# Optimization experiments

Hardware: AMD Instinct MI355X
Metric: run time of the kernel (lower is better)

Reference implementation:

```python
import jax, jax.numpy as jnp
import numpy as np

EPS = 1e-5
DC = 4  # conv kernel size


def _rmsnorm(x, w):
    return x * jax.lax.rsqrt(jnp.mean(x * x, axis=-1, keepdims=True) + EPS) * w


def _depthwise_causal_conv(x, w, b):
    # x: (B, L, ED), w: (ED, 1, DC), b: (ED,)
    xt = jnp.transpose(x, (0, 2, 1))  # (B, ED, L)
    y = jax.lax.conv_general_dilated(
        xt, w, window_strides=(1,), padding=[(DC - 1, 0)],
        feature_group_count=w.shape[0], dimension_numbers=("NCH", "OIH", "NCH"))
    y = y + b[None, :, None]
    return jnp.transpose(y, (0, 2, 1))  # (B, L, ED)


def _mamba_block(x, in_w, cw, cb, xp_w, dt_w, dt_b, A_log, Dp, out_w):
    B, L, _ = x.shape
    ED, N = A_log.shape
    dt_rank = dt_w.shape[1]
    xz = jnp.einsum('bld,ed->ble', x, in_w)          # (B, L, 2*ED)
    xi, z = jnp.split(xz, 2, axis=-1)
    xi = jax.nn.silu(_depthwise_causal_conv(xi, cw, cb))  # (B, L, ED)
    dbc = jnp.einsum('ble,fe->blf', xi, xp_w)        # (B, L, dt_rank+2N)
    delta, Bm, Cm = jnp.split(dbc, [dt_rank, dt_rank + N], axis=-1)
    delta = jax.nn.softplus(jnp.einsum('blr,er->ble', delta, dt_w) + dt_b)  # (B,L,ED)
    A = -jnp.exp(A_log)                              # (ED, N)
    dA = jnp.exp(delta[..., None] * A)               # (B, L, ED, N)
    dBx = delta[..., None] * Bm[:, :, None, :] * xi[..., None]  # (B, L, ED, N)

    def step(h, inp):
        a, bx = inp
        h = a * h + bx
        return h, h

    h0 = jnp.zeros((B, ED, N), x.dtype)
    _, hs = jax.lax.scan(step, h0, (jnp.moveaxis(dA, 1, 0), jnp.moveaxis(dBx, 1, 0)))
    y = jnp.einsum('lbdn,bln->bld', hs, Cm) + Dp * xi  # (B, L, ED)
    y = y * jax.nn.silu(z)
    return jnp.einsum('ble,de->bld', y, out_w)


def setup_inputs() -> dict:
    key = jax.random.key(0)
    ks = jax.random.split(key, 12)
    B, L, Dm, NL, ED, N, R = 16, 2048, 64, 4, 128, 16, 4
    s = 0.05
    A = jnp.tile(jnp.log(jnp.arange(1, N + 1, dtype=jnp.float32))[None, None, :], (NL, ED, 1))
    return {
        "x": jax.random.normal(ks[0], (B, L, Dm), jnp.float32),
        "norm_w": jnp.ones((NL, Dm), jnp.float32),
        "in_proj_w": jax.random.normal(ks[1], (NL, 2 * ED, Dm), jnp.float32) * s,
        "conv_w": jax.random.normal(ks[2], (NL, ED, 1, DC), jnp.float32) * 0.2,
        "conv_b": jnp.zeros((NL, ED), jnp.float32),
        "x_proj_w": jax.random.normal(ks[3], (NL, R + 2 * N, ED), jnp.float32) * s,
        "dt_proj_w": jax.random.normal(ks[4], (NL, ED, R), jnp.float32) * s,
        "dt_proj_b": jnp.full((NL, ED), -4.0, jnp.float32),
        "A_log": A,
        "D_skip": jnp.ones((NL, ED), jnp.float32),
        "out_proj_w": jax.random.normal(ks[5], (NL, Dm, ED), jnp.float32) * s,
        "fc_w": jax.random.normal(ks[6], (Dm, Dm), jnp.float32) * s,
        "fc_b": jnp.zeros((Dm,), jnp.float32),
    }


def reference(x, norm_w, in_proj_w, conv_w, conv_b, x_proj_w, dt_proj_w,
              dt_proj_b, A_log, D_skip, out_proj_w, fc_w, fc_b):
    n_layers = norm_w.shape[0]
    for l in range(n_layers):
        x = x + _mamba_block(_rmsnorm(x, norm_w[l]), in_proj_w[l], conv_w[l],
                             conv_b[l], x_proj_w[l], dt_proj_w[l], dt_proj_b[l],
                             A_log[l], D_skip[l], out_proj_w[l])
    last = x[:, -1, :]
    return jnp.einsum('bd,od->bo', last, fc_w) + fc_b
```

## Files before the change

kernel.cpp:

```cpp
#include <hip/hip_runtime.h>
#include <math.h>

#define B_   16
#define L_   2048
#define DM   64
#define NL_  4
#define ED_  128
#define NS   16
#define RK   4
#define BL   (B_*L_)
#define CHUNKS 128
#define CHLEN  (L_/CHUNKS)
#define SEQS   (B_*ED_*NS)

__device__ __forceinline__ void pow_chain16(float r, float* p) {
  float r2 = r * r, r4 = r2 * r2, r8 = r4 * r4;
  p[0]=r;      p[1]=r2;      p[2]=r2*r;    p[3]=r4;
  p[4]=r4*r;   p[5]=r4*r2;   p[6]=r4*p[2]; p[7]=r8;
  p[8]=r8*r;   p[9]=r8*r2;   p[10]=r8*p[2];p[11]=r8*r4;
  p[12]=r8*p[4];p[13]=r8*p[5];p[14]=r8*p[6];p[15]=r8*r8;
}

__global__ __launch_bounds__(256) void gemm_in_rms_k(const float* __restrict__ X,
    const float* __restrict__ nw, const float* __restrict__ W, float* __restrict__ XZ)
{
  __shared__ float4 sX[64][17];
  __shared__ float4 sW[16][64];
  int tid = threadIdx.x;
  int row0 = blockIdx.x * 64;
  int col0 = blockIdx.y * 64;
  const float* Wh = W + (size_t)col0 * 64;
#pragma unroll
  for (int it = 0; it < 4; it++) {
    int i = tid + it * 256;
    int r = i >> 4, q = i & 15;
    float4 v = *(const float4*)(X + (size_t)(row0 + r) * 64 + q * 4);
    float ss = v.x*v.x + v.y*v.y + v.z*v.z + v.w*v.w;
    ss += __shfl_xor(ss, 1, 16);
    ss += __shfl_xor(ss, 2, 16);
    ss += __shfl_xor(ss, 4, 16);
    ss += __shfl_xor(ss, 8, 16);
    float sc = rsqrtf(ss * (1.0f/64.0f) + 1e-5f);
    float4 wv = *(const float4*)(nw + q * 4);
    float4 o;
    o.x = v.x*sc*wv.x; o.y = v.y*sc*wv.y; o.z = v.z*sc*wv.z; o.w = v.w*sc*wv.w;
    sX[r][q] = o;
  }
#pragma unroll
  for (int it = 0; it < 4; it++) {
    int i = tid + it * 256;
    int c = i >> 4, k4 = i & 15;
    sW[k4][c] = *(const float4*)(Wh + (size_t)c * 64 + k4 * 4);
  }
  __syncthreads();
  int rg = tid >> 4;
  int cg = tid & 15;
  float acc[4][4];
#pragma unroll
  for (int i = 0; i < 4; i++)
#pragma unroll
    for (int j = 0; j < 4; j++) acc[i][j] = 0.f;
  for (int k4 = 0; k4 < 16; k4++) {
    float4 x[4];
#pragma unroll
    for (int i = 0; i < 4; i++) x[i] = sX[4*rg + i][k4];
#pragma unroll
    for (int j = 0; j < 4; j++) {
      float4 wv = sW[k4][cg + 16*j];
#pragma unroll
      for (int i = 0; i < 4; i++) {
        acc[i][j] = fmaf(x[i].x,wv.x, fmaf(x[i].y,wv.y,
                    fmaf(x[i].z,wv.z, fmaf(x[i].w,wv.w, acc[i][j]))));
      }
    }
  }
#pragma unroll
  for (int i = 0; i < 4; i++) {
#pragma unroll
    for (int j = 0; j < 4; j++) {
      XZ[(size_t)(row0 + 4*rg + i) * 256 + col0 + cg + 16*j] = acc[i][j];
    }
  }
}

__global__ __launch_bounds__(512) void convdbc_scan1_k(const float* __restrict__ XZ,
    const float* __restrict__ cw, const float* __restrict__ cb,
    const float* __restrict__ W,
    const float* __restrict__ dtw, const float* __restrict__ dtb,
    const float* __restrict__ alog,
    float* __restrict__ XI, float* __restrict__ DBC,
    float* __restrict__ AP, float* __restrict__ HZ)
{
  __shared__ float4 sX[64][33];
  __shared__ float4 sW[32][40];
  __shared__ __align__(16) float sDBC[64*40];
  int tid = threadIdx.x;
  int row0 = blockIdx.x * 64;
  int l0 = row0 & (L_ - 1);
  int b  = row0 >> 11;
#pragma unroll
  for (int it = 0; it < 4; it++) {
    int i = tid + it * 512;
    int r = i >> 5, k4 = i & 31;
    int l = l0 + r;
    const float* base = XZ + (size_t)(row0 + r) * 256 + k4 * 4;
    float4 z4 = make_float4(0.f,0.f,0.f,0.f);
    float4 t3 = (l >= 3) ? *(const float4*)(base - 3*256) : z4;
    float4 t2 = (l >= 2) ? *(const float4*)(base - 2*256) : z4;
    float4 t1 = (l >= 1) ? *(const float4*)(base - 1*256) : z4;
    float4 t0 = *(const float4*)(base);
    float4 w0 = *(const float4*)(cw + (k4*4+0)*4);
    float4 w1 = *(const float4*)(cw + (k4*4+1)*4);
    float4 w2 = *(const float4*)(cw + (k4*4+2)*4);
    float4 w3 = *(const float4*)(cw + (k4*4+3)*4);
    float4 bb = *(const float4*)(cb + k4*4);
    float4 o;
    o.x = fmaf(t3.x,w0.x, fmaf(t2.x,w0.y, fmaf(t1.x,w0.z, fmaf(t0.x,w0.w, bb.x))));
    o.y = fmaf(t3.y,w1.x, fmaf(t2.y,w1.y, fmaf(t1.y,w1.z, fmaf(t0.y,w1.w, bb.y))));
    o.z = fmaf(t3.z,w2.x, fmaf(t2.z,w2.y, fmaf(t1.z,w2.z, fmaf(t0.z,w2.w, bb.z))));
    o.w = fmaf(t3.w,w3.x, fmaf(t2.w,w3.y, fmaf(t1.w,w3.z, fmaf(t0.w,w3.w, bb.w))));
    o.x = o.x / (1.f + __expf(-o.x));
    o.y = o.y / (1.f + __expf(-o.y));
    o.z = o.z / (1.f + __expf(-o.z));
    o.w = o.w / (1.f + __expf(-o.w));
    sX[r][k4] = o;
    *(float4*)(XI + (size_t)(row0 + r) * 128 + k4 * 4) = o;
  }
  for (int i = tid; i < 36 * 32; i += 512) {
    int f = i >> 5, k4 = i & 31;
    sW[k4][f] = *(const float4*)(W + (size_t)f * 128 + k4 * 4);
  }
  __syncthreads();
  {
    int r  = tid >> 3;
    int cg = tid & 7;
    float acc[5];
#pragma unroll
    for (int j = 0; j < 5; j++) acc[j] = 0.f;
    for (int k4 = 0; k4 < 32; k4++) {
      float4 x0 = sX[r][k4];
#pragma unroll
      for (int j = 0; j < 5; j++) {
        float4 wv = sW[k4][cg + 8*j];
        acc[j] = fmaf(x0.x,wv.x, fmaf(x0.y,wv.y, fmaf(x0.z,wv.z, fmaf(x0.w,wv.w, acc[j]))));
      }
    }
#pragma unroll
    for (int j = 0; j < 5; j++) {
      int c = cg + 8*j;
      if (c < 36) {
        DBC[(size_t)(row0 + r) * 36 + c] = acc[j];
        sDBC[r*40 + c] = acc[j];
      }
    }
  }
  __syncthreads();
  {
    int e = tid & 127;
    int q = tid >> 7;
    float a[NS];
#pragma unroll
    for (int n = 0; n < NS; n++) a[n] = -__expf(alog[e*NS + n]);
    bool fast = true;
#pragma unroll
    for (int n = 0; n < NS; n++) fast = fast && (fabsf(a[n] + (float)(n+1)) <= 1e-3f);
    float4 w4 = *(const float4*)(dtw + e*4);
    float bias = dtb[e];
    const float* sXf = (const float*)sX;
    float h[NS];
#pragma unroll
    for (int n = 0; n < NS; n++) h[n] = 0.f;
    float Ssum = 0.f;
    for (int t = 0; t < CHLEN; t++) {
      int r = q * CHLEN + t;
      const float* dr = sDBC + r * 40;
      float4 d4 = *(const float4*)dr;
      float pre = fmaf(d4.x,w4.x, fmaf(d4.y,w4.y, fmaf(d4.z,w4.z, fmaf(d4.w,w4.w, bias))));
      float ex = __expf(pre);
      float delta = (pre > 20.f) ? pre : __logf(1.f + ex);
      Ssum += delta;
      float xi = sXf[r * 132 + e];
      float dx = delta * xi;
      float4 b0 = *(const float4*)(dr + 4);
      float4 b1 = *(const float4*)(dr + 8);
      float4 b2 = *(const float4*)(dr + 12);
      float4 b3 = *(const float4*)(dr + 16);
      float Bv[NS] = {b0.x,b0.y,b0.z,b0.w, b1.x,b1.y,b1.z,b1.w,
                      b2.x,b2.y,b2.z,b2.w, b3.x,b3.y,b3.z,b3.w};
      float p[NS];
      if (fast) {
        pow_chain16(__expf(-delta), p);
      } else {
#pragma unroll
        for (int n = 0; n < NS; n++) p[n] = __expf(delta * a[n]);
      }
#pragma unroll
      for (int n = 0; n < NS; n++) h[n] = fmaf(p[n], h[n], dx * Bv[n]);
    }
    float ap[NS];
    if (fast) {
      pow_chain16(__expf(-Ssum), ap);
    } else {
#pragma unroll
      for (int n = 0; n < NS; n++) ap[n] = __expf(a[n] * Ssum);
    }
    int ch = (l0 >> 4) + q;
    size_t base = (size_t)ch * SEQS + ((size_t)(b * ED_ + e)) * NS;
#pragma unroll
    for (int i = 0; i < 4; i++) {
      *(float4*)(AP + base + i*4) = make_float4(ap[4*i], ap[4*i+1], ap[4*i+2], ap[4*i+3]);
      *(float4*)(HZ + base + i*4) = make_float4(h[4*i],  h[4*i+1],  h[4*i+2],  h[4*i+3]);
    }
  }
}

__global__ __launch_bounds__(256) void scan_combine_k(const float* __restrict__ AP,
    const float* __restrict__ HZ, float* __restrict__ HI)
{
  __shared__ float sA[CHUNKS * 33];
  __shared__ float sH[CHUNKS * 33];
  int tid = threadIdx.x;
  int t0 = blockIdx.x * 32;
  for (int i = tid; i < CHUNKS * 32; i += 256) {
    int ch = i >> 5, s = i & 31;
    sA[ch*33 + s] = AP[(size_t)ch * SEQS + t0 + s];
    sH[ch*33 + s] = HZ[(size_t)ch * SEQS + t0 + s];
  }
  __syncthreads();
  int lane = tid & 63;
  int wid = tid >> 6;
  for (int j = 0; j < 8; j++) {
    int s = wid * 8 + j;
    float a0 = sA[(2*lane)*33 + s],   h0 = sH[(2*lane)*33 + s];
    float a1 = sA[(2*lane+1)*33 + s], h1 = sH[(2*lane+1)*33 + s];
    float aL = a0 * a1;
    float hL = fmaf(a1, h0, h1);
#pragma unroll
    for (int off = 1; off < 64; off <<= 1) {
      float aP = __shfl_up(aL, off, 64);
      float hP = __shfl_up(hL, off, 64);
      if (lane >= off) { hL = fmaf(aL, hP, hL); aL = aP * aL; }
    }
    float hPrev = __shfl_up(hL, 1, 64);
    if (lane == 0) hPrev = 0.f;
    sA[(2*lane)*33 + s]   = hPrev;
    sA[(2*lane+1)*33 + s] = fmaf(a0, hPrev, h0);
  }
  __syncthreads();
  for (int i = tid; i < CHUNKS * 32; i += 256) {
    int ch = i >> 5, s = i & 31;
    HI[(size_t)ch * SEQS + t0 + s] = sA[ch*33 + s];
  }
}

__global__ __launch_bounds__(512) void pass2_out_k(
    const float* __restrict__ DBC_, const float* __restrict__ XI_,
    const float* __restrict__ XZ,
    const float* __restrict__ dtw, const float* __restrict__ dtb,
    const float* __restrict__ alog, const float* __restrict__ Dp_,
    const float* __restrict__ HI,
    const float* __restrict__ Wo, const float* __restrict__ XOLD,
    float* __restrict__ XNEW)
{
  __shared__ __align__(16) float sYX[64 * 132];
  __shared__ float4 sWo[64][33];
  __shared__ __align__(16) float sDBC[64*40];
  int tid = threadIdx.x;
  int row0 = blockIdx.x * 64;
  int b   = row0 >> 11;
  int ch0 = (row0 & (L_ - 1)) >> 4;
#pragma unroll
  for (int it = 0; it < 4; it++) {
    int i = tid + it * 512;
    int o = i >> 5, k4 = i & 31;
    sWo[o][k4] = *(const float4*)(Wo + (size_t)o * 128 + k4 * 4);
  }
#pragma unroll
  for (int it = 0; it < 16; it++) {
    int i = tid + it * 512;
    int r = i >> 7, e = i & 127;
    sYX[r * 132 + e] = XI_[(size_t)row0 * 128 + i];
  }
  for (int i = tid; i < 64 * 36; i += 512) {
    sDBC[(i / 36) * 40 + (i % 36)] = DBC_[(size_t)row0 * 36 + i];
  }
  __syncthreads();
  {
    int e  = tid & 127;
    int q  = tid >> 7;
    int ch = ch0 + q;
    float a[NS];
#pragma unroll
    for (int n = 0; n < NS; n++) a[n] = -__expf(alog[e*NS + n]);
    bool fast = true;
#pragma unroll
    for (int n = 0; n < NS; n++) fast = fast && (fabsf(a[n] + (float)(n+1)) <= 1e-3f);
    float4 w4 = *(const float4*)(dtw + e*4);
    float bias = dtb[e];
    float Dp = Dp_[e];
    size_t sbase = (size_t)ch * SEQS + ((size_t)(b * ED_ + e)) * NS;
    float h[NS];
#pragma unroll
    for (int i = 0; i < 4; i++) {
      float4 v = *(const float4*)(HI + sbase + i*4);
      h[4*i] = v.x; h[4*i+1] = v.y; h[4*i+2] = v.z; h[4*i+3] = v.w;
    }
    for (int t = 0; t < CHLEN; t++) {
      int r = q * CHLEN + t;
      int bl = b * L_ + ch * CHLEN + t;
      const float* dr = sDBC + r * 40;
      float4 d4 = *(const float4*)dr;
      float pre = fmaf(d4.x,w4.x, fmaf(d4.y,w4.y, fmaf(d4.z,w4.z, fmaf(d4.w,w4.w, bias))));
      float ex = __expf(pre);
      float delta = (pre > 20.f) ? pre : __logf(1.f + ex);
      float xi = sYX[r * 132 + e];
      float dx = delta * xi;
      float4 b0 = *(const float4*)(dr + 4);
      float4 b1 = *(const float4*)(dr + 8);
      float4 b2 = *(const float4*)(dr + 12);
      float4 b3 = *(const float4*)(dr + 16);
      float4 c0 = *(const float4*)(dr + 20);
      float4 c1 = *(const float4*)(dr + 24);
      float4 c2 = *(const float4*)(dr + 28);
      float4 c3 = *(const float4*)(dr + 32);
      float Bv[NS] = {b0.x,b0.y,b0.z,b0.w, b1.x,b1.y,b1.z,b1.w,
                      b2.x,b2.y,b2.z,b2.w, b3.x,b3.y,b3.z,b3.w};
      float Cv[NS] = {c0.x,c0.y,c0.z,c0.w, c1.x,c1.y,c1.z,c1.w,
                      c2.x,c2.y,c2.z,c2.w, c3.x,c3.y,c3.z,c3.w};
      float p[NS];
      if (fast) {
        pow_chain16(__expf(-delta), p);
      } else {
#pragma unroll
        for (int n = 0; n < NS; n++) p[n] = __expf(delta * a[n]);
      }
      float y = 0.f;
#pragma unroll
      for (int n = 0; n < NS; n++) {
        h[n] = fmaf(p[n], h[n], dx * Bv[n]);
        y = fmaf(h[n], Cv[n], y);
      }
      y = fmaf(Dp, xi, y);
      float z = XZ[(size_t)bl * 256 + 128 + e];
      float sz = z / (1.f + __expf(-z));
      sYX[r * 132 + e] = y * sz;
    }
  }
  __syncthreads();
  {
    int r2 = tid >> 4;
    int og = tid & 15;
    const float4* sY0 = (const float4*)(sYX + (2*r2    ) * 132);
    const float4* sY1 = (const float4*)(sYX + (2*r2 + 1) * 132);
    float acc0[4], acc1[4];
#pragma unroll
    for (int j = 0; j < 4; j++) { acc0[j] = 0.f; acc1[j] = 0.f; }
    for (int k4 = 0; k4 < 32; k4++) {
      float4 y0 = sY0[k4];
      float4 y1 = sY1[k4];
#pragma unroll
      for (int j = 0; j < 4; j++) {
        float4 wv = sWo[og + 16*j][k4];
        acc0[j] = fmaf(y0.x,wv.x, fmaf(y0.y,wv.y, fmaf(y0.z,wv.z, fmaf(y0.w,wv.w, acc0[j]))));
        acc1[j] = fmaf(y1.x,wv.x, fmaf(y1.y,wv.y, fmaf(y1.z,wv.z, fmaf(y1.w,wv.w, acc1[j]))));
      }
    }
#pragma unroll
    for (int j = 0; j < 4; j++) {
      int o = og + 16*j;
      size_t i0 = (size_t)(row0 + 2*r2    ) * 64 + o;
      size_t i1 = (size_t)(row0 + 2*r2 + 1) * 64 + o;
      XNEW[i0] = XOLD[i0] + acc0[j];
      XNEW[i1] = XOLD[i1] + acc1[j];
    }
  }
}

__global__ __launch_bounds__(256) void final_k(const float* __restrict__ X,
    const float* __restrict__ fcw, const float* __restrict__ fcb, float* __restrict__ out)
{
  int t = blockIdx.x * 256 + threadIdx.x;
  int b = t >> 6, o = t & 63;
  const float* xrow = X + ((size_t)b * L_ + (L_ - 1)) * 64;
  const float* wrow = fcw + o * 64;
  float acc = fcb[o];
#pragma unroll
  for (int d = 0; d < 64; d++) acc = fmaf(xrow[d], wrow[d], acc);
  out[t] = acc;
}

extern "C" void kernel_launch(void* const* d_in, const int* in_sizes, int n_in,
                              void* d_out, int out_size, void* d_ws, size_t ws_size,
                              hipStream_t stream)
{
  const float* x_in   = (const float*)d_in[0];
  const float* norm_w = (const float*)d_in[1];
  const float* in_w   = (const float*)d_in[2];
  const float* conv_w = (const float*)d_in[3];
  const float* conv_b = (const float*)d_in[4];
  const float* xp_w   = (const float*)d_in[5];
  const float* dt_w   = (const float*)d_in[6];
  const float* dt_b   = (const float*)d_in[7];
  const float* A_log  = (const float*)d_in[8];
  const float* D_skip = (const float*)d_in[9];
  const float* out_w  = (const float*)d_in[10];
  const float* fc_w   = (const float*)d_in[11];
  const float* fc_b   = (const float*)d_in[12];
  float* out = (float*)d_out;

  float* ws  = (float*)d_ws;
  float* X   = ws;
  float* XZ  = X   + (size_t)BL*64;
  float* XI  = XZ  + (size_t)BL*256;
  float* DBC = XI  + (size_t)BL*128;
  float* AP  = DBC + (size_t)BL*36;
  float* HZ  = AP  + (size_t)CHUNKS*SEQS;
  float* HI  = HZ  + (size_t)CHUNKS*SEQS;

  for (int l = 0; l < NL_; l++) {
    const float* xsrc = (l == 0) ? x_in : X;
    gemm_in_rms_k<<<dim3(BL/64, 4), 256, 0, stream>>>(xsrc, norm_w + l*DM,
                    in_w + (size_t)l*2*ED_*DM, XZ);
    convdbc_scan1_k<<<BL/64, 512, 0, stream>>>(XZ, conv_w + l*ED_*4, conv_b + l*ED_,
                    xp_w + (size_t)l*36*ED_,
                    dt_w + l*ED_*RK, dt_b + l*ED_, A_log + l*ED_*NS,
                    XI, DBC, AP, HZ);
    scan_combine_k<<<SEQS/32, 256, 0, stream>>>(AP, HZ, HI);
    pass2_out_k<<<BL/64, 512, 0, stream>>>(DBC, XI, XZ,
                    dt_w + l*ED_*RK, dt_b + l*ED_, A_log + l*ED_*NS, D_skip + l*ED_,
                    HI, out_w + (size_t)l*DM*ED_, xsrc, X);
  }
  final_k<<<4, 256, 0, stream>>>(X, fc_w, fc_b, out);
}
```

Before: 392.1 us.

## Fuse next layer's RMSNorm and in-projection into pass2 output epilogue

The pass2 kernel now applies the next layer's RMSNorm to the fresh residual rows it has just produced and computes the next layer's in-projection GEMM. It does the norm with a 16-lane shuffle reduction and stages the weight in reused shared memory, writing XZ directly. The standalone gemm_in_rms kernel now runs only for layer 0. This removes three kernel launches and a global re-read of the residual stream. In exchange pass2 takes on more work per block, and it overwrites XZ in place, which relies on each block only reading its own rows.

Result: no change. 388.8 us (-0.8%).

```diff
diff --git a/kernel.cpp b/kernel.cpp
--- a/kernel.cpp
+++ b/kernel.cpp
@@ -260,7 +260,9 @@
     const float* __restrict__ alog, const float* __restrict__ Dp_,
     const float* __restrict__ HI,
     const float* __restrict__ Wo, const float* __restrict__ XOLD,
-    float* __restrict__ XNEW)
+    float* __restrict__ XNEW,
+    int doNext, const float* __restrict__ nw_next,
+    const float* __restrict__ W_next, float* __restrict__ XZn)
 {
   __shared__ __align__(16) float sYX[64 * 132];
   __shared__ float4 sWo[64][33];
@@ -347,9 +349,10 @@
     }
   }
   __syncthreads();
+  int r2 = tid >> 4;
+  int og = tid & 15;
+  float v0[4], v1[4];
   {
-    int r2 = tid >> 4;
-    int og = tid & 15;
     const float4* sY0 = (const float4*)(sYX + (2*r2    ) * 132);
     const float4* sY1 = (const float4*)(sYX + (2*r2 + 1) * 132);
     float acc0[4], acc1[4];
@@ -370,8 +373,63 @@
       int o = og + 16*j;
       size_t i0 = (size_t)(row0 + 2*r2    ) * 64 + o;
       size_t i1 = (size_t)(row0 + 2*r2 + 1) * 64 + o;
-      XNEW[i0] = XOLD[i0] + acc0[j];
-      XNEW[i1] = XOLD[i1] + acc1[j];
+      v0[j] = XOLD[i0] + acc0[j];
+      v1[j] = XOLD[i1] + acc1[j];
+      XNEW[i0] = v0[j];
+      XNEW[i1] = v1[j];
+    }
+  }
+  if (doNext) {
+    float ss0 = 0.f, ss1 = 0.f;
+#pragma unroll
+    for (int j = 0; j < 4; j++) { ss0 += v0[j]*v0[j]; ss1 += v1[j]*v1[j]; }
+    ss0 += __shfl_xor(ss0, 1, 16); ss0 += __shfl_xor(ss0, 2, 16);
+    ss0 += __shfl_xor(ss0, 4, 16); ss0 += __shfl_xor(ss0, 8, 16);
+    ss1 += __shfl_xor(ss1, 1, 16); ss1 += __shfl_xor(ss1, 2, 16);
+    ss1 += __shfl_xor(ss1, 4, 16); ss1 += __shfl_xor(ss1, 8, 16);
+    float sc0 = rsqrtf(ss0 * (1.0f/64.0f) + 1e-5f);
+    float sc1 = rsqrtf(ss1 * (1.0f/64.0f) + 1e-5f);
+    __syncthreads();
+    float* sXNf = sYX;
+    float4 (*sW16)[128] = (float4(*)[128])sWo;
+#pragma unroll
+    for (int j = 0; j < 4; j++) {
+      int c = og + 16*j;
+      float nwv = nw_next[c];
+      sXNf[(2*r2    )*68 + c] = v0[j]*sc0*nwv;
+      sXNf[(2*r2 + 1)*68 + c] = v1[j]*sc1*nwv;
+    }
+    __syncthreads();
+    for (int half = 0; half < 2; half++) {
+#pragma unroll
+      for (int it = 0; it < 4; it++) {
+        int i = tid + it * 512;
+        int c = i >> 4, k4 = i & 15;
+        sW16[k4][c] = *(const float4*)(W_next + (size_t)(half*128 + c) * 64 + k4 * 4);
+      }
+      __syncthreads();
+      const float4* xr0 = (const float4*)(sXNf + (2*r2    ) * 68);
+      const float4* xr1 = (const float4*)(sXNf + (2*r2 + 1) * 68);
+      float a0[8], a1[8];
+#pragma unroll
+      for (int j = 0; j < 8; j++) { a0[j] = 0.f; a1[j] = 0.f; }
+      for (int k4 = 0; k4 < 16; k4++) {
+        float4 x0 = xr0[k4];
+        float4 x1 = xr1[k4];
+#pragma unroll
+        for (int j = 0; j < 8; j++) {
+          float4 wv = sW16[k4][og + 16*j];
+          a0[j] = fmaf(x0.x,wv.x, fmaf(x0.y,wv.y, fmaf(x0.z,wv.z, fmaf(x0.w,wv.w, a0[j]))));
+          a1[j] = fmaf(x1.x,wv.x, fmaf(x1.y,wv.y, fmaf(x1.z,wv.z, fmaf(x1.w,wv.w, a1[j]))));
+        }
+      }
+#pragma unroll
+      for (int j = 0; j < 8; j++) {
+        int c = half*128 + og + 16*j;
+        XZn[(size_t)(row0 + 2*r2    ) * 256 + c] = a0[j];
+        XZn[(size_t)(row0 + 2*r2 + 1) * 256 + c] = a1[j];
+      }
+      if (half == 0) __syncthreads();
     }
   }
 }
@@ -419,16 +477,21 @@
 
   for (int l = 0; l < NL_; l++) {
     const float* xsrc = (l == 0) ? x_in : X;
-    gemm_in_rms_k<<<dim3(BL/64, 4), 256, 0, stream>>>(xsrc, norm_w + l*DM,
-                    in_w + (size_t)l*2*ED_*DM, XZ);
+    if (l == 0) {
+      gemm_in_rms_k<<<dim3(BL/64, 4), 256, 0, stream>>>(x_in, norm_w,
+                      in_w, XZ);
+    }
     convdbc_scan1_k<<<BL/64, 512, 0, stream>>>(XZ, conv_w + l*ED_*4, conv_b + l*ED_,
                     xp_w + (size_t)l*36*ED_,
                     dt_w + l*ED_*RK, dt_b + l*ED_, A_log + l*ED_*NS,
                     XI, DBC, AP, HZ);
     scan_combine_k<<<SEQS/32, 256, 0, stream>>>(AP, HZ, HI);
+    int doNext = (l < NL_ - 1) ? 1 : 0;
+    int ln = (l < NL_ - 1) ? (l + 1) : l;
     pass2_out_k<<<BL/64, 512, 0, stream>>>(DBC, XI, XZ,
                     dt_w + l*ED_*RK, dt_b + l*ED_, A_log + l*ED_*NS, D_skip + l*ED_,
-                    HI, out_w + (size_t)l*DM*ED_, xsrc, X);
+                    HI, out_w + (size_t)l*DM*ED_, xsrc, X,
+                    doNext, norm_w + ln*DM, in_w + (size_t)ln*2*ED_*DM, XZ);
   }
   final_k<<<4, 256, 0, stream>>>(X, fc_w, fc_b, out);
 }
```
